# Performance work log

Hardware: AMD Instinct MI355X
Metric: run time of the kernel (lower is better)

The kernel has to match this reference:

```python
import jax, jax.numpy as jnp
import numpy as np

TEMPERATURE = 0.5


def setup_inputs() -> dict:
    key = jax.random.key(0)
    k1, k2 = jax.random.split(key)
    N, Z = 4096, 2048
    z1 = jax.random.normal(k1, (N, Z), dtype=jnp.float32)
    z2 = jax.random.normal(k2, (N, Z), dtype=jnp.float32)
    return {"z1": z1, "z2": z2}


def reference(z1, z2):
    # NT-Xent loss. Original torch code: normalize, build full 2Nx2N cosine-sim
    # matrix, prepend the positive pair column, cross-entropy with label 0.
    # Mathematically, per-row CE with the positive prepended and the self-sim
    # removed equals: logsumexp over the row excluding the diagonal, minus the
    # positive logit.  (cosine_similarity on already-normalized vectors is a
    # plain dot product, so normalization is applied once.)
    n, _ = z1.shape
    a = z1 / jnp.linalg.norm(z1, axis=1, keepdims=True)  # [N, Z]
    b = z2 / jnp.linalg.norm(z2, axis=1, keepdims=True)  # [N, Z]
    reps = jnp.concatenate([a, b], axis=0)               # [2N, Z]
    logits = jnp.matmul(reps, reps.T) / TEMPERATURE      # [2N, 2N]
    NEG_INF = jnp.float32(-1e9)  # mask self-similarity (excluded from CE denom)
    logits = jnp.where(jnp.eye(2 * n, dtype=bool), NEG_INF, logits)
    pos = jnp.sum(a * b, axis=1) / TEMPERATURE           # [N] positive logits
    pos = jnp.concatenate([pos, pos])                    # [2N]
    lse = jax.nn.logsumexp(logits, axis=1)               # [2N]
    # sum of CE over 2N rows, divided by 2N  == mean
    return jnp.mean(lse - pos)
```

## Files before the change

kernel.cpp:

```cpp
#include <hip/hip_runtime.h>
#include <stdint.h>

#define N_ROWS 4096
#define Z_DIM  2048
#define TOT    8192
#define TILE   128
#define RBYTES (Z_DIM / 2)
#define BKE    128
#define KBYT   (BKE / 2)
#define NITER  (Z_DIM / BKE)
#define NT     (TOT / TILE)
#define NBLK   (NT * (NT + 1) / 2)
#define INV_T  2.0f
#define SCL4   64.0f

typedef __attribute__((ext_vector_type(4))) int   intx4;
typedef __attribute__((ext_vector_type(8))) int   intx8;
typedef __attribute__((ext_vector_type(4))) float floatx4;

#define GLOAD16(g, l)                                                   \
    __builtin_amdgcn_global_load_lds(                                   \
        (const __attribute__((address_space(1))) unsigned int*)(g),     \
        (__attribute__((address_space(3))) unsigned int*)(l), 16, 0, 0)

__device__ __forceinline__ unsigned int f2fp4(float v) {
    float a = fabsf(v);
    unsigned int c = (a >= 0.25f) + (a >= 0.75f) + (a >= 1.25f) + (a >= 1.75f)
                   + (a >= 2.5f)  + (a >= 3.5f)  + (a >= 5.0f);
    return c | (v < 0.f ? 8u : 0u);
}

__global__ __launch_bounds__(256) void normalize_kernel(
    const float* __restrict__ z1, const float* __restrict__ z2,
    unsigned char* __restrict__ reps, float* __restrict__ pos,
    float* __restrict__ rowsum)
{
    const int row  = blockIdx.x;
    const int tid  = threadIdx.x;
    const int lane = tid & 63, wave = tid >> 6;

    if (row < TOT / 256) rowsum[row * 256 + tid] = 0.f;

    const float4* p1 = (const float4*)(z1 + (size_t)row * Z_DIM);
    const float4* p2 = (const float4*)(z2 + (size_t)row * Z_DIM);
    float4 x0 = p1[tid * 2], x1 = p1[tid * 2 + 1];
    float4 y0 = p2[tid * 2], y1 = p2[tid * 2 + 1];

    float s1 = x0.x*x0.x + x0.y*x0.y + x0.z*x0.z + x0.w*x0.w
             + x1.x*x1.x + x1.y*x1.y + x1.z*x1.z + x1.w*x1.w;
    float s2 = y0.x*y0.x + y0.y*y0.y + y0.z*y0.z + y0.w*y0.w
             + y1.x*y1.x + y1.y*y1.y + y1.z*y1.z + y1.w*y1.w;
    float dd = x0.x*y0.x + x0.y*y0.y + x0.z*y0.z + x0.w*y0.w
             + x1.x*y1.x + x1.y*y1.y + x1.z*y1.z + x1.w*y1.w;

    #pragma unroll
    for (int m = 1; m < 64; m <<= 1) {
        s1 += __shfl_xor(s1, m);
        s2 += __shfl_xor(s2, m);
        dd += __shfl_xor(dd, m);
    }
    __shared__ float red[3][4];
    if (lane == 0) { red[0][wave] = s1; red[1][wave] = s2; red[2][wave] = dd; }
    __syncthreads();
    s1 = red[0][0] + red[0][1] + red[0][2] + red[0][3];
    s2 = red[1][0] + red[1][1] + red[1][2] + red[1][3];
    dd = red[2][0] + red[2][1] + red[2][2] + red[2][3];

    const float inv1 = rsqrtf(s1), inv2 = rsqrtf(s2);
    if (tid == 0) {
        float p = dd * inv1 * inv2 * INV_T;
        pos[row] = p;
        pos[row + N_ROWS] = p;
    }

    const float a = inv1 * SCL4, b = inv2 * SCL4;
    unsigned int pa =  f2fp4(x0.x * a)        | (f2fp4(x0.y * a) << 4)
                    | (f2fp4(x0.z * a) << 8)  | (f2fp4(x0.w * a) << 12)
                    | (f2fp4(x1.x * a) << 16) | (f2fp4(x1.y * a) << 20)
                    | (f2fp4(x1.z * a) << 24) | (f2fp4(x1.w * a) << 28);
    unsigned int pb =  f2fp4(y0.x * b)        | (f2fp4(y0.y * b) << 4)
                    | (f2fp4(y0.z * b) << 8)  | (f2fp4(y0.w * b) << 12)
                    | (f2fp4(y1.x * b) << 16) | (f2fp4(y1.y * b) << 20)
                    | (f2fp4(y1.z * b) << 24) | (f2fp4(y1.w * b) << 28);
    *(unsigned int*)(reps + (size_t)row * RBYTES + tid * 4) = pa;
    *(unsigned int*)(reps + (size_t)(N_ROWS + row) * RBYTES + tid * 4) = pb;
}

__global__ __launch_bounds__(256) void simclr_gemm(
    const unsigned char* __restrict__ reps, float* __restrict__ rowsum)
{
    __shared__ __align__(16) unsigned char L[3][2][TILE * KBYT];

    const int bid = blockIdx.x;
    const int t = (bid & 7) * (NBLK / 8) + (bid >> 3);
    int r = (int)((sqrtf(8.0f * (float)t + 1.0f) - 1.0f) * 0.5f);
    while ((r + 1) * (r + 2) / 2 <= t) ++r;
    while (r * (r + 1) / 2 > t) --r;
    const int bi = t - r * (r + 1) / 2;
    const int bj = r;
    const bool diag = (bi == bj);

    const int tid  = threadIdx.x;
    const int lane = tid & 63, wave = tid >> 6;
    const int wr = wave >> 1, wc = wave & 1;
    const int quad = lane >> 4, l16 = lane & 15;
    const int sw   = (l16 >> 1) & 3;
    const int row0 = bi * TILE, col0 = bj * TILE;

    floatx4 acc[4][4];
    #pragma unroll
    for (int i = 0; i < 4; ++i)
        #pragma unroll
        for (int j = 0; j < 4; ++j)
            acc[i][j] = floatx4{0.f, 0.f, 0.f, 0.f};

    const int c0 = tid, c1 = tid + 256;
    const int r0s = c0 >> 2, k0s = (c0 & 3) ^ ((r0s >> 1) & 3);
    const int r1s = c1 >> 2, k1s = (c1 & 3) ^ ((r1s >> 1) & 3);
    const unsigned char* gA0 = reps + (size_t)(row0 + r0s) * RBYTES + k0s * 16;
    const unsigned char* gA1 = reps + (size_t)(row0 + r1s) * RBYTES + k1s * 16;
    const unsigned char* gB0 = reps + (size_t)(col0 + r0s) * RBYTES + k0s * 16;
    const unsigned char* gB1 = reps + (size_t)(col0 + r1s) * RBYTES + k1s * 16;
    const int o0 = c0 * 16, o1 = c1 * 16;

    GLOAD16(gA0, &L[0][0][o0]);
    GLOAD16(gA1, &L[0][0][o1]);
    GLOAD16(gB0, &L[0][1][o0]);
    GLOAD16(gB1, &L[0][1][o1]);
    GLOAD16(gA0 + KBYT, &L[1][0][o0]);
    GLOAD16(gA1 + KBYT, &L[1][0][o1]);
    GLOAD16(gB0 + KBYT, &L[1][1][o0]);
    GLOAD16(gB1 + KBYT, &L[1][1][o1]);

    int cur = 0;
    #pragma unroll 1
    for (int i = 0; i < NITER; ++i) {
        if (i + 1 < NITER) asm volatile("s_waitcnt vmcnt(4)" ::: "memory");
        else               asm volatile("s_waitcnt vmcnt(0)" ::: "memory");
        __builtin_amdgcn_s_barrier();
        asm volatile("" ::: "memory");

        if (i + 2 < NITER) {
            const size_t ko = (size_t)(i + 2) * KBYT;
            int pf = cur + 2; if (pf >= 3) pf -= 3;
            GLOAD16(gA0 + ko, &L[pf][0][o0]);
            GLOAD16(gA1 + ko, &L[pf][0][o1]);
            GLOAD16(gB0 + ko, &L[pf][1][o0]);
            GLOAD16(gB1 + ko, &L[pf][1][o1]);
        }
        const unsigned char* Ab = &L[cur][0][0];
        const unsigned char* Bb = &L[cur][1][0];

        intx8 af[4], bf[4];
        #pragma unroll
        for (int fi = 0; fi < 4; ++fi) {
            const int ar = (wr * 64 + fi * 16 + l16) * KBYT;
            const int br = (wc * 64 + fi * 16 + l16) * KBYT;
            intx4 av = *(const intx4*)&Ab[ar + ((quad ^ sw) << 4)];
            intx4 bv = *(const intx4*)&Bb[br + ((quad ^ sw) << 4)];
            af[fi] = intx8{av[0], av[1], av[2], av[3], 0, 0, 0, 0};
            bf[fi] = intx8{bv[0], bv[1], bv[2], bv[3], 0, 0, 0, 0};
        }
        __builtin_amdgcn_s_setprio(1);
        #pragma unroll
        for (int fi = 0; fi < 4; ++fi)
            #pragma unroll
            for (int j = 0; j < 4; ++j)
                acc[fi][j] = __builtin_amdgcn_mfma_scale_f32_16x16x128_f8f6f4(
                    af[fi], bf[j], acc[fi][j],
                    4, 4,
                    0, 0x7F7F7F7Fu,
                    0, 0x7F7F7F7Fu);
        __builtin_amdgcn_s_setprio(0);
        cur = (cur == 2) ? 0 : cur + 1;
    }

    const float descale = INV_T / (SCL4 * SCL4);
    float scol[4] = {0.f, 0.f, 0.f, 0.f};
    #pragma unroll
    for (int fi = 0; fi < 4; ++fi) {
        const int rbase = row0 + wr * 64 + fi * 16 + quad * 4;
        float srow[4] = {0.f, 0.f, 0.f, 0.f};
        #pragma unroll
        for (int j = 0; j < 4; ++j) {
            const int c = col0 + wc * 64 + j * 16 + l16;
            #pragma unroll
            for (int rr = 0; rr < 4; ++rr) {
                float e = __expf(acc[fi][j][rr] * descale);
                if (diag && (rbase + rr == c)) e = 0.f;
                srow[rr] += e;
                scol[j]  += e;
            }
        }
        #pragma unroll
        for (int rr = 0; rr < 4; ++rr) {
            #pragma unroll
            for (int m = 1; m < 16; m <<= 1) srow[rr] += __shfl_xor(srow[rr], m);
        }
        if (l16 == 0) {
            #pragma unroll
            for (int rr = 0; rr < 4; ++rr)
                atomicAdd(&rowsum[rbase + rr], srow[rr]);
        }
    }
    if (!diag) {
        #pragma unroll
        for (int j = 0; j < 4; ++j) {
            scol[j] += __shfl_xor(scol[j], 16);
            scol[j] += __shfl_xor(scol[j], 32);
        }
        if (quad == 0) {
            #pragma unroll
            for (int j = 0; j < 4; ++j)
                atomicAdd(&rowsum[col0 + wc * 64 + j * 16 + l16], scol[j]);
        }
    }
}

__global__ __launch_bounds__(1024) void finalize_kernel(
    const float* __restrict__ rowsum, const float* __restrict__ pos,
    float* __restrict__ out)
{
    const int tid = threadIdx.x;
    const int lane = tid & 63, wave = tid >> 6;
    float s = 0.f;
    for (int r = tid; r < TOT; r += 1024) s += logf(rowsum[r]) - pos[r];
    #pragma unroll
    for (int m = 1; m < 64; m <<= 1) s += __shfl_xor(s, m);
    __shared__ float red[16];
    if (lane == 0) red[wave] = s;
    __syncthreads();
    if (tid == 0) {
        float t = 0.f;
        #pragma unroll
        for (int w = 0; w < 16; ++w) t += red[w];
        out[0] = t * (1.0f / TOT);
    }
}

extern "C" void kernel_launch(void* const* d_in, const int* in_sizes, int n_in,
                              void* d_out, int out_size, void* d_ws, size_t ws_size,
                              hipStream_t stream)
{
    const float* z1 = (const float*)d_in[0];
    const float* z2 = (const float*)d_in[1];
    float* out = (float*)d_out;

    char* w = (char*)d_ws;
    unsigned char* reps = (unsigned char*)w;
    float* pos    = (float*)(w + (size_t)TOT * RBYTES);
    float* rowsum = pos + TOT;

    normalize_kernel<<<N_ROWS, 256, 0, stream>>>(z1, z2, reps, pos, rowsum);
    simclr_gemm<<<NBLK, 256, 0, stream>>>(reps, rowsum);
    finalize_kernel<<<1, 1024, 0, stream>>>(rowsum, pos, out);
}
```

Baseline: 149.1 us.

## Cut GEMM LDS and registers: double-buffer B, stream A fragments, raise occupancy

The FP4 MFMA GEMM now keeps a triple buffer for A but only a double buffer for B in shared memory, reducing LDS per block. B is prefetched one step ahead and A two steps ahead. A fragments are loaded one at a time inside the MFMA loop into a single register vector instead of holding all four, and the upper halves of the fragment vectors stay zero for the whole loop. The kernel asks for 4 blocks per CU via launch bounds to raise occupancy. The price is less latency hiding for B and LDS reads interleaved with MFMAs, which can leave the matrix units waiting.

New measurement: 154.5 us. +3.7%, slower.

```diff
diff --git a/kernel.cpp b/kernel.cpp
--- a/kernel.cpp
+++ b/kernel.cpp
@@ -11,6 +11,7 @@
 #define NITER  (Z_DIM / BKE)
 #define NT     (TOT / TILE)
 #define NBLK   (NT * (NT + 1) / 2)
+#define OPB    (TILE * KBYT)
 #define INV_T  2.0f
 #define SCL4   64.0f
 
@@ -86,10 +87,11 @@
     *(unsigned int*)(reps + (size_t)(N_ROWS + row) * RBYTES + tid * 4) = pb;
 }
 
-__global__ __launch_bounds__(256) void simclr_gemm(
+__global__ __launch_bounds__(256, 4) void simclr_gemm(
     const unsigned char* __restrict__ reps, float* __restrict__ rowsum)
 {
-    __shared__ __align__(16) unsigned char L[3][2][TILE * KBYT];
+    __shared__ __align__(16) unsigned char LA[3][OPB];
+    __shared__ __align__(16) unsigned char LB[2][OPB];
 
     const int bid = blockIdx.x;
     const int t = (bid & 7) * (NBLK / 8) + (bid >> 3);
@@ -114,65 +116,71 @@
         for (int j = 0; j < 4; ++j)
             acc[i][j] = floatx4{0.f, 0.f, 0.f, 0.f};
 
-    const int c0 = tid, c1 = tid + 256;
-    const int r0s = c0 >> 2, k0s = (c0 & 3) ^ ((r0s >> 1) & 3);
-    const int r1s = c1 >> 2, k1s = (c1 & 3) ^ ((r1s >> 1) & 3);
+    const int r0s = tid >> 2, k0s = (tid & 3) ^ ((r0s >> 1) & 3);
     const unsigned char* gA0 = reps + (size_t)(row0 + r0s) * RBYTES + k0s * 16;
-    const unsigned char* gA1 = reps + (size_t)(row0 + r1s) * RBYTES + k1s * 16;
     const unsigned char* gB0 = reps + (size_t)(col0 + r0s) * RBYTES + k0s * 16;
-    const unsigned char* gB1 = reps + (size_t)(col0 + r1s) * RBYTES + k1s * 16;
-    const int o0 = c0 * 16, o1 = c1 * 16;
-
-    GLOAD16(gA0, &L[0][0][o0]);
-    GLOAD16(gA1, &L[0][0][o1]);
-    GLOAD16(gB0, &L[0][1][o0]);
-    GLOAD16(gB1, &L[0][1][o1]);
-    GLOAD16(gA0 + KBYT, &L[1][0][o0]);
-    GLOAD16(gA1 + KBYT, &L[1][0][o1]);
-    GLOAD16(gB0 + KBYT, &L[1][1][o0]);
-    GLOAD16(gB1 + KBYT, &L[1][1][o1]);
-
-    int cur = 0;
+    const int o0 = tid * 16;
+
+    intx8 a8 = intx8{0, 0, 0, 0, 0, 0, 0, 0};
+    intx8 b8[4];
+    #pragma unroll
+    for (int j = 0; j < 4; ++j) b8[j] = intx8{0, 0, 0, 0, 0, 0, 0, 0};
+
+    GLOAD16(gA0,                     &LA[0][o0]);
+    GLOAD16(gA0 + 64 * RBYTES,       &LA[0][o0 + 4096]);
+    GLOAD16(gB0,                     &LB[0][o0]);
+    GLOAD16(gB0 + 64 * RBYTES,       &LB[0][o0 + 4096]);
+    GLOAD16(gA0 + KBYT,              &LA[1][o0]);
+    GLOAD16(gA0 + 64 * RBYTES + KBYT, &LA[1][o0 + 4096]);
+
+    int bufA = 0;
     #pragma unroll 1
     for (int i = 0; i < NITER; ++i) {
-        if (i + 1 < NITER) asm volatile("s_waitcnt vmcnt(4)" ::: "memory");
+        if (i + 1 < NITER) asm volatile("s_waitcnt vmcnt(2)" ::: "memory");
         else               asm volatile("s_waitcnt vmcnt(0)" ::: "memory");
         __builtin_amdgcn_s_barrier();
         asm volatile("" ::: "memory");
 
+        if (i + 1 < NITER) {
+            const size_t ko = (size_t)(i + 1) * KBYT;
+            unsigned char* d = &LB[(i + 1) & 1][0];
+            GLOAD16(gB0 + ko,               d + o0);
+            GLOAD16(gB0 + 64 * RBYTES + ko, d + o0 + 4096);
+        }
+        asm volatile("" ::: "memory");
         if (i + 2 < NITER) {
             const size_t ko = (size_t)(i + 2) * KBYT;
-            int pf = cur + 2; if (pf >= 3) pf -= 3;
-            GLOAD16(gA0 + ko, &L[pf][0][o0]);
-            GLOAD16(gA1 + ko, &L[pf][0][o1]);
-            GLOAD16(gB0 + ko, &L[pf][1][o0]);
-            GLOAD16(gB1 + ko, &L[pf][1][o1]);
-        }
-        const unsigned char* Ab = &L[cur][0][0];
-        const unsigned char* Bb = &L[cur][1][0];
-
-        intx8 af[4], bf[4];
+            int pf = bufA + 2; if (pf >= 3) pf -= 3;
+            unsigned char* d = &LA[pf][0];
+            GLOAD16(gA0 + ko,               d + o0);
+            GLOAD16(gA0 + 64 * RBYTES + ko, d + o0 + 4096);
+        }
+
+        const unsigned char* Ab = &LA[bufA][0];
+        const unsigned char* Bb = &LB[i & 1][0];
+
+        #pragma unroll
+        for (int j = 0; j < 4; ++j)
+            *(intx4*)&b8[j] =
+                *(const intx4*)&Bb[(wc * 64 + j * 16 + l16) * KBYT
+                                   + ((quad ^ sw) << 4)];
+
+        __builtin_amdgcn_s_setprio(1);
         #pragma unroll
         for (int fi = 0; fi < 4; ++fi) {
-            const int ar = (wr * 64 + fi * 16 + l16) * KBYT;
-            const int br = (wc * 64 + fi * 16 + l16) * KBYT;
-            intx4 av = *(const intx4*)&Ab[ar + ((quad ^ sw) << 4)];
-            intx4 bv = *(const intx4*)&Bb[br + ((quad ^ sw) << 4)];
-            af[fi] = intx8{av[0], av[1], av[2], av[3], 0, 0, 0, 0};
-            bf[fi] = intx8{bv[0], bv[1], bv[2], bv[3], 0, 0, 0, 0};
-        }
-        __builtin_amdgcn_s_setprio(1);
-        #pragma unroll
-        for (int fi = 0; fi < 4; ++fi)
+            *(intx4*)&a8 =
+                *(const intx4*)&Ab[(wr * 64 + fi * 16 + l16) * KBYT
+                                   + ((quad ^ sw) << 4)];
             #pragma unroll
             for (int j = 0; j < 4; ++j)
                 acc[fi][j] = __builtin_amdgcn_mfma_scale_f32_16x16x128_f8f6f4(
-                    af[fi], bf[j], acc[fi][j],
+                    a8, b8[j], acc[fi][j],
                     4, 4,
                     0, 0x7F7F7F7Fu,
                     0, 0x7F7F7F7Fu);
+        }
         __builtin_amdgcn_s_setprio(0);
-        cur = (cur == 2) ? 0 : cur + 1;
+        bufA = (bufA == 2) ? 0 : bufA + 1;
     }
 
     const float descale = INV_T / (SCL4 * SCL4);
```
